# Kernel tuning notes

Measured on AMD Instinct MI355X. Metric: run time of the kernel, lower is better.

Reference implementation:

```python
import jax, jax.numpy as jnp
import numpy as np

OBS = 4096      # flattened observation size (hardcoded in down_sampler)
ENC = 1024      # encoding_size
LAT = 512       # policy_latent_size
ACT = 3         # action_space_n
B = 4096        # batch
NMAX = 8        # max neighbors (padded ragged dim)


def setup_inputs() -> dict:
    key = jax.random.key(0)
    ks = jax.random.split(key, 16)

    def w(i, shape, fan_in):
        return jax.random.normal(ks[i], shape, jnp.float32) * (1.0 / np.sqrt(fan_in))

    return {
        "observation": jax.random.normal(ks[0], (B, OBS), jnp.float32),
        "neighbors": jax.random.normal(ks[1], (B, NMAX, LAT), jnp.float32),
        "neighbor_counts": jax.random.randint(ks[2], (B,), 0, 9, jnp.int32),
        # down_sampler: Linear(4096, ENC) + ReLU
        "W_ds": w(3, (ENC, OBS), OBS), "b_ds": jnp.zeros((ENC,), jnp.float32),
        # policy: Linear(ENC, LAT) + ReLU
        "W_pol": w(4, (LAT, ENC), ENC), "b_pol": jnp.zeros((LAT,), jnp.float32),
        # v_net: Linear(ENC, 1) + Tanh
        "W_v": w(5, (1, ENC), ENC), "b_v": jnp.zeros((1,), jnp.float32),
        # GRUCell(LAT, LAT): weight_ih [3L, L], weight_hh [3L, L]
        "W_ih": w(6, (3 * LAT, LAT), LAT), "b_ih": jnp.zeros((3 * LAT,), jnp.float32),
        "W_hh": w(7, (3 * LAT, LAT), LAT), "b_hh": jnp.zeros((3 * LAT,), jnp.float32),
        # to_probs: Linear(LAT, ACT) + ReLU + Softmax
        "W_pr": w(8, (ACT, LAT), LAT), "b_pr": jnp.zeros((ACT,), jnp.float32),
    }


def _gru_cell(x, h, W_ih, b_ih, W_hh, b_hh):
    # PyTorch GRUCell semantics; gates ordered (r, z, n)
    gi = x @ W_ih.T + b_ih          # [B, 3L]
    gh = h @ W_hh.T + b_hh          # [B, 3L]
    i_r, i_z, i_n = jnp.split(gi, 3, axis=-1)
    h_r, h_z, h_n = jnp.split(gh, 3, axis=-1)
    r = jax.nn.sigmoid(i_r + h_r)
    z = jax.nn.sigmoid(i_z + h_z)
    n = jnp.tanh(i_n + r * h_n)
    return (1.0 - z) * n + z * h


def reference(observation, neighbors, neighbor_counts,
              W_ds, b_ds, W_pol, b_pol, W_v, b_v,
              W_ih, b_ih, W_hh, b_hh, W_pr, b_pr):
    # step 0: forward_initial
    enc = jax.nn.relu(observation @ W_ds.T + b_ds)        # [B, ENC]
    pol = jax.nn.relu(enc @ W_pol.T + b_pol)              # [B, LAT]
    state_vals = jnp.tanh(enc @ W_v.T + b_v)              # [B, 1]

    # step 1: forward_communicate -- ragged GRU recurrence over padded neighbors
    xs = jnp.swapaxes(neighbors, 0, 1)                    # [NMAX, B, LAT]
    ts = jnp.arange(NMAX)

    def step(h, xt):
        x, t = xt
        h_new = _gru_cell(x, h, W_ih, b_ih, W_hh, b_hh)
        valid = (t < neighbor_counts)[:, None]            # mask padded neighbor slots
        return jnp.where(valid, h_new, h), None

    h, _ = jax.lax.scan(step, pol, (xs, ts))              # [B, LAT]

    # step 2: forward_probs
    probs = jax.nn.softmax(jax.nn.relu(h @ W_pr.T + b_pr), axis=-1)  # [B, ACT]
    return probs, state_vals
```

## Files before the change

### kernel.cpp

```cpp
#include <hip/hip_runtime.h>
#include <hip/hip_bf16.h>

typedef __attribute__((ext_vector_type(8))) short short8;
typedef __attribute__((ext_vector_type(4))) float floatx4;

__device__ __forceinline__ ushort f2bf(float x) {
    unsigned u = __float_as_uint(x);
    unsigned r = (u + 0x7fffu + ((u >> 16) & 1u)) >> 16;
    return (ushort)r;
}
__device__ __forceinline__ float bf2f(ushort h) {
    return __uint_as_float(((unsigned)h) << 16);
}
__device__ __forceinline__ float fast_sigmoid(float x) {
    return 1.0f / (1.0f + __expf(-x));
}
__device__ __forceinline__ float fast_tanh(float x) {
    x = fminf(fmaxf(x, -15.0f), 15.0f);
    float e = __expf(2.0f * x);
    return (e - 1.0f) / (e + 1.0f);
}
__device__ __forceinline__ void load_lds16(const void* g, void* l) {
    __builtin_amdgcn_global_load_lds(
        (__attribute__((address_space(1))) void*)(g),
        (__attribute__((address_space(3))) void*)(l),
        16, 0, 0);
}

__device__ __forceinline__ void stage_unit(const ushort* grow0, int ld, ushort* lds_unit) {
    const int lane = threadIdx.x & 63;
    const int r = lane >> 3;
    const int c = (lane & 7) ^ r;
    load_lds16(grow0 + (size_t)r * ld + c * 8, lds_unit);
}
__device__ __forceinline__ short8 lds_read8(const ushort* buf, int R, int c_el) {
    const int idx = ((R >> 3) << 9) + ((R & 7) << 6) + ((((c_el >> 3) ^ (R & 7))) << 3);
    return *(const short8*)(buf + idx);
}

__global__ __launch_bounds__(256) void cvt_f32_bf16(const float* __restrict__ src,
                                                    ushort* __restrict__ dst, int n4) {
    int i = blockIdx.x * blockDim.x + threadIdx.x;
    if (i >= n4) return;
    const float4 v = ((const float4*)src)[i];
    ushort4 o;
    o.x = f2bf(v.x); o.y = f2bf(v.y); o.z = f2bf(v.z); o.w = f2bf(v.w);
    ((ushort4*)dst)[i] = o;
}

__global__ __launch_bounds__(256) void sort_by_cnt(const int* __restrict__ cnt,
                                                   int* __restrict__ perm,
                                                   int* __restrict__ inv,
                                                   int* __restrict__ nact) {
    __shared__ int h[9];
    __shared__ int cur[9];
    const int tid = threadIdx.x;
    if (tid < 9) h[tid] = 0;
    __syncthreads();
    for (int i = tid; i < 4096; i += 256) atomicAdd(&h[cnt[i]], 1);
    __syncthreads();
    if (tid == 0) {
        int off = 0;
        for (int c = 8; c >= 0; --c) { cur[c] = off; off += h[c]; }
        for (int t = 0; t < 8; ++t) {
            int n = 0;
            for (int c = t + 1; c <= 8; ++c) n += h[c];
            nact[t] = n;
        }
    }
    __syncthreads();
    for (int i = tid; i < 4096; i += 256) {
        const int c = cnt[i];
        const int p = atomicAdd(&cur[c], 1);
        perm[p] = i;
        inv[i] = p;
    }
}

template <int MODE, int BN, int KSPLIT, bool MAP>
__global__ __launch_bounds__(256, 2) void gemm64(
    const ushort* __restrict__ A, int lda,
    const ushort* __restrict__ B, int ldb,
    const float* __restrict__ bias,
    const int* __restrict__ row_map,
    ushort* __restrict__ Cb, float* __restrict__ Cf, int ldc,
    int K, size_t part_stride) {
    __shared__ __attribute__((aligned(16))) ushort sA[64 * 64];
    __shared__ __attribute__((aligned(16))) ushort sB[BN * 64];

    constexpr int NJ = (BN + 63) / 64;
    constexpr int UB = BN / 32;

    const int tid = threadIdx.x;
    const int lane = tid & 63;
    const int w = tid >> 6;
    const int m0 = blockIdx.y * 64;
    const int n0 = blockIdx.x * BN;
    const int wn = w * (16 * NJ);
    const int nl = lane & 15;

    const int Kper = K / KSPLIT;
    const int kbase = (KSPLIT > 1) ? blockIdx.z * Kper : 0;
    if (MODE == 3) Cf += (size_t)blockIdx.z * part_stride;

    floatx4 acc[4][NJ] = {};

    for (int k0 = kbase; k0 < kbase + Kper; k0 += 64) {
#pragma unroll
        for (int u = 0; u < 2; ++u) {
            const int ua = w * 2 + u;
            stage_unit(A + (size_t)(m0 + ua * 8) * lda + k0, lda, &sA[ua * 512]);
        }
#pragma unroll
        for (int u = 0; u < UB; ++u) {
            const int ub = w * UB + u;
            stage_unit(B + (size_t)(n0 + ub * 8) * ldb + k0, ldb, &sB[ub * 512]);
        }
        __syncthreads();
#pragma unroll
        for (int kk = 0; kk < 2; ++kk) {
            const int cb = kk * 32 + (lane >> 4) * 8;
            short8 a[4], b[NJ];
#pragma unroll
            for (int i = 0; i < 4; ++i) a[i] = lds_read8(sA, i * 16 + nl, cb);
#pragma unroll
            for (int j = 0; j < NJ; ++j) b[j] = lds_read8(sB, wn + j * 16 + nl, cb);
#pragma unroll
            for (int i = 0; i < 4; ++i)
#pragma unroll
                for (int j = 0; j < NJ; ++j)
                    acc[i][j] = __builtin_amdgcn_mfma_f32_16x16x32_bf16(a[i], b[j], acc[i][j], 0, 0, 0);
        }
        __syncthreads();
    }

    const int ml = (lane >> 4) * 4;
#pragma unroll
    for (int j = 0; j < NJ; ++j) {
        const int n = n0 + wn + j * 16 + nl;
        float bv = 0.0f;
        if (MODE == 2) bv = bias[n];
#pragma unroll
        for (int i = 0; i < 4; ++i) {
            const int mbase = m0 + i * 16 + ml;
#pragma unroll
            for (int r = 0; r < 4; ++r) {
                float v = acc[i][j][r];
                const int mr = mbase + r;
                const int orow = MAP ? row_map[mr] : mr;
                const size_t off = (size_t)orow * ldc + n;
                if (MODE == 2) {
                    v += bv; v = fmaxf(v, 0.0f);
                    Cb[off] = f2bf(v);
                    Cf[off] = v;
                } else {
                    Cf[off] = v;
                }
            }
        }
    }
}

__global__ __launch_bounds__(256) void combine_relu(const float* __restrict__ p0,
                                                    const float* __restrict__ p1,
                                                    const float* __restrict__ bias,
                                                    ushort* __restrict__ ob, int n4) {
    int i = blockIdx.x * blockDim.x + threadIdx.x;
    if (i >= n4) return;
    const float4 a = ((const float4*)p0)[i];
    const float4 b = ((const float4*)p1)[i];
    const int col = (i * 4) & 1023;
    const float4 bs = *(const float4*)(bias + col);
    ushort4 o;
    o.x = f2bf(fmaxf(a.x + b.x + bs.x, 0.f));
    o.y = f2bf(fmaxf(a.y + b.y + bs.y, 0.f));
    o.z = f2bf(fmaxf(a.z + b.z + bs.z, 0.f));
    o.w = f2bf(fmaxf(a.w + b.w + bs.w, 0.f));
    ((ushort4*)ob)[i] = o;
}

__global__ __launch_bounds__(256, 2) void gru_step(
    const ushort* __restrict__ Xall,
    const ushort* __restrict__ Hin,
    const ushort* __restrict__ Wih,
    const ushort* __restrict__ Whh,
    const float* __restrict__ bih, const float* __restrict__ bhh,
    const int* __restrict__ perm, const int* __restrict__ nact,
    float* __restrict__ hf, ushort* __restrict__ Hout, int t) {
    __shared__ __attribute__((aligned(16))) ushort sX[64 * 64];
    __shared__ __attribute__((aligned(16))) ushort sH[64 * 64];
    __shared__ __attribute__((aligned(16))) ushort sBih[192 * 64];
    __shared__ __attribute__((aligned(16))) ushort sBhh[192 * 64];

    const int tid = threadIdx.x;
    const int lane = tid & 63;
    const int w = tid >> 6;
    const int s = blockIdx.x;
    const int m0 = blockIdx.y * 64;
    const int na = nact[t];

    if (m0 >= na) {
        const int rr = tid >> 2;
        const size_t base = (size_t)(m0 + rr) * 512 + s * 64;
        const uint4* src = (const uint4*)(Hin + base);
        uint4* dst = (uint4*)(Hout + base);
        const int cc = (tid & 3) * 2;
        dst[cc] = src[cc];
        dst[cc + 1] = src[cc + 1];
        return;
    }

    const int nl = lane & 15;
    const int ml = (lane >> 4) * 4;
    const int col = s * 64 + w * 16 + nl;

    const int r = lane >> 3;
    const int c = (lane & 7) ^ r;
    const ushort* X = Xall + t * 512;
    const ushort* xb[2];
    const ushort* hbp[2];
#pragma unroll
    for (int u = 0; u < 2; ++u) {
        const int srow = m0 + (w * 2 + u) * 8 + r;
        const int orig = perm[srow];
        xb[u] = X + (size_t)orig * 4096 + c * 8;
        hbp[u] = Hin + (size_t)srow * 512 + c * 8;
    }
    const ushort* wi[6];
    const ushort* wh[6];
#pragma unroll
    for (int j = 0; j < 6; ++j) {
        const int u = w * 6 + j;
        const int grow = (u >> 3) * 512 + s * 64 + (u & 7) * 8 + r;
        wi[j] = Wih + (size_t)grow * 512 + c * 8;
        wh[j] = Whh + (size_t)grow * 512 + c * 8;
    }

    floatx4 accr[4], accz[4], accn[4], acch[4];
    {
        const float br_ = bih[col] + bhh[col];
        const float bz_ = bih[512 + col] + bhh[512 + col];
        const float bn_i = bih[1024 + col];
        const float bn_h = bhh[1024 + col];
        const floatx4 vr = {br_, br_, br_, br_};
        const floatx4 vz = {bz_, bz_, bz_, bz_};
        const floatx4 vi = {bn_i, bn_i, bn_i, bn_i};
        const floatx4 vh = {bn_h, bn_h, bn_h, bn_h};
#pragma unroll
        for (int i = 0; i < 4; ++i) { accr[i] = vr; accz[i] = vz; accn[i] = vi; acch[i] = vh; }
    }

    for (int k0 = 0; k0 < 512; k0 += 64) {
#pragma unroll
        for (int u = 0; u < 2; ++u) {
            const int ua = w * 2 + u;
            load_lds16(xb[u] + k0, &sX[ua * 512]);
            load_lds16(hbp[u] + k0, &sH[ua * 512]);
        }
#pragma unroll
        for (int j = 0; j < 6; ++j) {
            const int u = w * 6 + j;
            load_lds16(wi[j] + k0, &sBih[u * 512]);
            load_lds16(wh[j] + k0, &sBhh[u * 512]);
        }
        __syncthreads();
#pragma unroll
        for (int kk = 0; kk < 2; ++kk) {
            const int cb = kk * 32 + (lane >> 4) * 8;
            short8 ax[4], ah[4];
#pragma unroll
            for (int i = 0; i < 4; ++i) {
                ax[i] = lds_read8(sX, i * 16 + nl, cb);
                ah[i] = lds_read8(sH, i * 16 + nl, cb);
            }
            const short8 bir = lds_read8(sBih, w * 16 + nl, cb);
            const short8 biz = lds_read8(sBih, 64 + w * 16 + nl, cb);
            const short8 bin = lds_read8(sBih, 128 + w * 16 + nl, cb);
            const short8 bhr = lds_read8(sBhh, w * 16 + nl, cb);
            const short8 bhz = lds_read8(sBhh, 64 + w * 16 + nl, cb);
            const short8 bhn = lds_read8(sBhh, 128 + w * 16 + nl, cb);
#pragma unroll
            for (int i = 0; i < 4; ++i) {
                accr[i] = __builtin_amdgcn_mfma_f32_16x16x32_bf16(ax[i], bir, accr[i], 0, 0, 0);
                accr[i] = __builtin_amdgcn_mfma_f32_16x16x32_bf16(ah[i], bhr, accr[i], 0, 0, 0);
                accz[i] = __builtin_amdgcn_mfma_f32_16x16x32_bf16(ax[i], biz, accz[i], 0, 0, 0);
                accz[i] = __builtin_amdgcn_mfma_f32_16x16x32_bf16(ah[i], bhz, accz[i], 0, 0, 0);
                accn[i] = __builtin_amdgcn_mfma_f32_16x16x32_bf16(ax[i], bin, accn[i], 0, 0, 0);
                acch[i] = __builtin_amdgcn_mfma_f32_16x16x32_bf16(ah[i], bhn, acch[i], 0, 0, 0);
            }
        }
        __syncthreads();
    }

    const bool full = (m0 + 64 <= na);
#pragma unroll
    for (int i = 0; i < 4; ++i) {
#pragma unroll
        for (int r4 = 0; r4 < 4; ++r4) {
            const int lr = i * 16 + ml + r4;
            const int row = m0 + lr;
            const float rg = fast_sigmoid(accr[i][r4]);
            const float zg = fast_sigmoid(accz[i][r4]);
            const float ng = fast_tanh(accn[i][r4] + rg * acch[i][r4]);
            const size_t off = (size_t)row * 512 + col;
            const float ho = hf[off];
            const bool act = full || (row < na);
            const float hv = act ? ((1.0f - zg) * ng + zg * ho) : ho;
            hf[off] = hv;
            Hout[off] = f2bf(hv);
        }
    }
}

__global__ __launch_bounds__(256) void v_kernel(const ushort* __restrict__ enc,
                                                const float* __restrict__ Wv,
                                                const float* __restrict__ bv,
                                                float* __restrict__ out) {
    const int row = blockIdx.x * 4 + (threadIdx.x >> 6);
    const int lane = threadIdx.x & 63;
    const ushort* e = enc + (size_t)row * 1024;
    float s = 0.0f;
#pragma unroll
    for (int i = 0; i < 16; ++i) {
        int k = lane + i * 64;
        s += bf2f(e[k]) * Wv[k];
    }
#pragma unroll
    for (int off = 32; off; off >>= 1) s += __shfl_down(s, off, 64);
    if (lane == 0) out[row] = fast_tanh(s + bv[0]);
}

__global__ __launch_bounds__(256) void probs_kernel(const float* __restrict__ h,
                                                    const float* __restrict__ Wpr,
                                                    const float* __restrict__ bpr,
                                                    const int* __restrict__ perm,
                                                    float* __restrict__ out) {
    const int srow = blockIdx.x * 4 + (threadIdx.x >> 6);
    const int lane = threadIdx.x & 63;
    const float* hr = h + (size_t)srow * 512;
    float p0 = 0.f, p1 = 0.f, p2 = 0.f;
#pragma unroll
    for (int i = 0; i < 8; ++i) {
        int k = lane + i * 64;
        float x = hr[k];
        p0 += x * Wpr[k];
        p1 += x * Wpr[512 + k];
        p2 += x * Wpr[1024 + k];
    }
#pragma unroll
    for (int off = 32; off; off >>= 1) {
        p0 += __shfl_down(p0, off, 64);
        p1 += __shfl_down(p1, off, 64);
        p2 += __shfl_down(p2, off, 64);
    }
    if (lane == 0) {
        const int orow = perm[srow];
        p0 = fmaxf(p0 + bpr[0], 0.f);
        p1 = fmaxf(p1 + bpr[1], 0.f);
        p2 = fmaxf(p2 + bpr[2], 0.f);
        float m = fmaxf(p0, fmaxf(p1, p2));
        float e0 = __expf(p0 - m), e1 = __expf(p1 - m), e2 = __expf(p2 - m);
        float inv = 1.0f / (e0 + e1 + e2);
        out[orow * 3 + 0] = e0 * inv;
        out[orow * 3 + 1] = e1 * inv;
        out[orow * 3 + 2] = e2 * inv;
    }
}

extern "C" void kernel_launch(void* const* d_in, const int* in_sizes, int n_in,
                              void* d_out, int out_size, void* d_ws, size_t ws_size,
                              hipStream_t stream) {
    const float* obs   = (const float*)d_in[0];
    const float* nbr   = (const float*)d_in[1];
    const int*   cnt   = (const int*)d_in[2];
    const float* W_ds  = (const float*)d_in[3];
    const float* b_ds  = (const float*)d_in[4];
    const float* W_pol = (const float*)d_in[5];
    const float* b_pol = (const float*)d_in[6];
    const float* W_v   = (const float*)d_in[7];
    const float* b_v   = (const float*)d_in[8];
    const float* W_ih  = (const float*)d_in[9];
    const float* b_ih  = (const float*)d_in[10];
    const float* W_hh  = (const float*)d_in[11];
    const float* b_hh  = (const float*)d_in[12];
    const float* W_pr  = (const float*)d_in[13];
    const float* b_pr  = (const float*)d_in[14];
    float* out = (float*)d_out;

    ushort* obs_b  = (ushort*)d_ws;
    ushort* Wds_b  = obs_b + 16777216;
    ushort* Wpol_b = Wds_b + 4194304;
    ushort* Wih_b  = Wpol_b + 524288;
    ushort* Whh_b  = Wih_b + 786432;
    ushort* enc_b  = Whh_b + 786432;
    ushort* h_b0   = enc_b + 4194304;
    ushort* h_b1   = h_b0 + 2097152;
    float*  h_f    = (float*)(h_b1 + 2097152);
    float*  part   = h_f + 2097152;
    ushort* nbr_b  = (ushort*)part;
    int*    perm   = (int*)(part + 8388608);
    int*    inv    = perm + 4096;
    int*    nact   = inv + 4096;

    sort_by_cnt<<<1, 256, 0, stream>>>(cnt, perm, inv, nact);

    cvt_f32_bf16<<<16384, 256, 0, stream>>>(obs, obs_b, 4194304);
    cvt_f32_bf16<<<4096, 256, 0, stream>>>(W_ds, Wds_b, 1048576);
    cvt_f32_bf16<<<512, 256, 0, stream>>>(W_pol, Wpol_b, 131072);
    cvt_f32_bf16<<<768, 256, 0, stream>>>(W_ih, Wih_b, 196608);
    cvt_f32_bf16<<<768, 256, 0, stream>>>(W_hh, Whh_b, 196608);

    gemm64<3, 128, 2, false><<<dim3(8, 64, 2), 256, 0, stream>>>(
        obs_b, 4096, Wds_b, 4096, nullptr, nullptr, nullptr, part, 1024, 4096, 4194304);
    combine_relu<<<4096, 256, 0, stream>>>(part, part + 4194304, b_ds, enc_b, 1048576);

    cvt_f32_bf16<<<16384, 256, 0, stream>>>(nbr, nbr_b, 4194304);

    gemm64<2, 64, 1, true><<<dim3(8, 64, 1), 256, 0, stream>>>(
        enc_b, 1024, Wpol_b, 1024, b_pol, inv, h_b0, h_f, 512, 1024, 0);

    v_kernel<<<1024, 256, 0, stream>>>(enc_b, W_v, b_v, out + 12288);

    for (int t = 0; t < 8; ++t) {
        const ushort* hin = (t & 1) ? h_b1 : h_b0;
        ushort* hout = (t & 1) ? h_b0 : h_b1;
        gru_step<<<dim3(8, 64), 256, 0, stream>>>(nbr_b, hin, Wih_b, Whh_b,
                                                  b_ih, b_hh, perm, nact, h_f, hout, t);
    }

    probs_kernel<<<1024, 256, 0, stream>>>(h_f, W_pr, b_pr, perm, out);
}
```

Measured before the change: 440.8 us.

## Split GRU input projection into separate GEMM and drop split-K in encoder GEMM

The encoder GEMM stops using split-K with a separate combine/ReLU kernel. It now runs a single full-K pass that fuses bias, ReLU and the bf16 store, with a block-index swizzle to improve cache locality. The GRU step is split in two: a per-step gi_gemm computes the input projection into an fp32 buffer aliased over the dead obs workspace, and gru_step does only the hidden projection plus the gates, using less LDS and higher occupancy. This trades eight extra launches and fp32 gi traffic for lighter recurrent kernels and the removal of the partial-sum round trip.

New measurement: 506.1 us. +14.8%, slower.

```diff
diff --git a/kernel.cpp b/kernel.cpp
--- a/kernel.cpp
+++ b/kernel.cpp
@@ -77,35 +77,40 @@
     }
 }
 
-template <int MODE, int BN, int KSPLIT, bool MAP>
+template <int MODE, int BN, bool MAP, bool SWZ>
 __global__ __launch_bounds__(256, 2) void gemm64(
     const ushort* __restrict__ A, int lda,
     const ushort* __restrict__ B, int ldb,
     const float* __restrict__ bias,
     const int* __restrict__ row_map,
     ushort* __restrict__ Cb, float* __restrict__ Cf, int ldc,
-    int K, size_t part_stride) {
+    int K) {
     __shared__ __attribute__((aligned(16))) ushort sA[64 * 64];
     __shared__ __attribute__((aligned(16))) ushort sB[BN * 64];
 
     constexpr int NJ = (BN + 63) / 64;
     constexpr int UB = BN / 32;
+
+    int bx = blockIdx.x, by = blockIdx.y;
+    if (SWZ) {
+        const int nwg = gridDim.x * gridDim.y;
+        const int b = by * gridDim.x + bx;
+        const int f = (b & 7) * (nwg >> 3) + (b >> 3);
+        bx = f % gridDim.x;
+        by = f / gridDim.x;
+    }
 
     const int tid = threadIdx.x;
     const int lane = tid & 63;
     const int w = tid >> 6;
-    const int m0 = blockIdx.y * 64;
-    const int n0 = blockIdx.x * BN;
+    const int m0 = by * 64;
+    const int n0 = bx * BN;
     const int wn = w * (16 * NJ);
     const int nl = lane & 15;
 
-    const int Kper = K / KSPLIT;
-    const int kbase = (KSPLIT > 1) ? blockIdx.z * Kper : 0;
-    if (MODE == 3) Cf += (size_t)blockIdx.z * part_stride;
-
     floatx4 acc[4][NJ] = {};
 
-    for (int k0 = kbase; k0 < kbase + Kper; k0 += 64) {
+    for (int k0 = 0; k0 < K; k0 += 64) {
 #pragma unroll
         for (int u = 0; u < 2; ++u) {
             const int ua = w * 2 + u;
@@ -138,59 +143,105 @@
 #pragma unroll
     for (int j = 0; j < NJ; ++j) {
         const int n = n0 + wn + j * 16 + nl;
-        float bv = 0.0f;
-        if (MODE == 2) bv = bias[n];
+        const float bv = bias[n];
 #pragma unroll
         for (int i = 0; i < 4; ++i) {
             const int mbase = m0 + i * 16 + ml;
 #pragma unroll
             for (int r = 0; r < 4; ++r) {
-                float v = acc[i][j][r];
+                float v = acc[i][j][r] + bv;
+                v = fmaxf(v, 0.0f);
                 const int mr = mbase + r;
                 const int orow = MAP ? row_map[mr] : mr;
                 const size_t off = (size_t)orow * ldc + n;
-                if (MODE == 2) {
-                    v += bv; v = fmaxf(v, 0.0f);
-                    Cb[off] = f2bf(v);
-                    Cf[off] = v;
-                } else {
-                    Cf[off] = v;
-                }
+                Cb[off] = f2bf(v);
+                if (MODE == 2) Cf[off] = v;
             }
         }
     }
 }
 
-__global__ __launch_bounds__(256) void combine_relu(const float* __restrict__ p0,
-                                                    const float* __restrict__ p1,
-                                                    const float* __restrict__ bias,
-                                                    ushort* __restrict__ ob, int n4) {
-    int i = blockIdx.x * blockDim.x + threadIdx.x;
-    if (i >= n4) return;
-    const float4 a = ((const float4*)p0)[i];
-    const float4 b = ((const float4*)p1)[i];
-    const int col = (i * 4) & 1023;
-    const float4 bs = *(const float4*)(bias + col);
-    ushort4 o;
-    o.x = f2bf(fmaxf(a.x + b.x + bs.x, 0.f));
-    o.y = f2bf(fmaxf(a.y + b.y + bs.y, 0.f));
-    o.z = f2bf(fmaxf(a.z + b.z + bs.z, 0.f));
-    o.w = f2bf(fmaxf(a.w + b.w + bs.w, 0.f));
-    ((ushort4*)ob)[i] = o;
-}
-
-__global__ __launch_bounds__(256, 2) void gru_step(
+__global__ __launch_bounds__(256, 4) void gi_gemm(
     const ushort* __restrict__ Xall,
+    const ushort* __restrict__ Wih,
+    const float* __restrict__ bih,
+    const int* __restrict__ perm, const int* __restrict__ nact,
+    float* __restrict__ gi, int t) {
+    __shared__ __attribute__((aligned(16))) ushort sA[64 * 64];
+    __shared__ __attribute__((aligned(16))) ushort sB[128 * 64];
+
+    const int m0 = blockIdx.y * 64;
+    if (m0 >= nact[t]) return;
+
+    const int tid = threadIdx.x;
+    const int lane = tid & 63;
+    const int w = tid >> 6;
+    const int n0 = blockIdx.x * 128;
+    const int wn = w * 32;
+    const int nl = lane & 15;
+
+    const int r = lane >> 3;
+    const int c = (lane & 7) ^ r;
+    const ushort* xb[2];
+#pragma unroll
+    for (int u = 0; u < 2; ++u) {
+        const int srow = m0 + (w * 2 + u) * 8 + r;
+        xb[u] = Xall + (size_t)perm[srow] * 4096 + t * 512 + c * 8;
+    }
+
+    floatx4 acc[4][2] = {};
+
+    for (int k0 = 0; k0 < 512; k0 += 64) {
+#pragma unroll
+        for (int u = 0; u < 2; ++u) load_lds16(xb[u] + k0, &sA[(w * 2 + u) * 512]);
+#pragma unroll
+        for (int u = 0; u < 4; ++u) {
+            const int ub = w * 4 + u;
+            stage_unit(Wih + (size_t)(n0 + ub * 8) * 512 + k0, 512, &sB[ub * 512]);
+        }
+        __syncthreads();
+#pragma unroll
+        for (int kk = 0; kk < 2; ++kk) {
+            const int cb = kk * 32 + (lane >> 4) * 8;
+            short8 a[4], b[2];
+#pragma unroll
+            for (int i = 0; i < 4; ++i) a[i] = lds_read8(sA, i * 16 + nl, cb);
+#pragma unroll
+            for (int j = 0; j < 2; ++j) b[j] = lds_read8(sB, wn + j * 16 + nl, cb);
+#pragma unroll
+            for (int i = 0; i < 4; ++i)
+#pragma unroll
+                for (int j = 0; j < 2; ++j)
+                    acc[i][j] = __builtin_amdgcn_mfma_f32_16x16x32_bf16(a[i], b[j], acc[i][j], 0, 0, 0);
+        }
+        __syncthreads();
+    }
+
+    const int ml = (lane >> 4) * 4;
+#pragma unroll
+    for (int j = 0; j < 2; ++j) {
+        const int n = n0 + wn + j * 16 + nl;
+        const float bv = bih[n];
+#pragma unroll
+        for (int i = 0; i < 4; ++i) {
+#pragma unroll
+            for (int r4 = 0; r4 < 4; ++r4) {
+                const int row = m0 + i * 16 + ml + r4;
+                gi[(size_t)row * 1536 + n] = acc[i][j][r4] + bv;
+            }
+        }
+    }
+}
+
+__global__ __launch_bounds__(256, 4) void gru_step(
     const ushort* __restrict__ Hin,
-    const ushort* __restrict__ Wih,
     const ushort* __restrict__ Whh,
-    const float* __restrict__ bih, const float* __restrict__ bhh,
-    const int* __restrict__ perm, const int* __restrict__ nact,
+    const float* __restrict__ bhh,
+    const int* __restrict__ nact,
+    const float* __restrict__ gi,
     float* __restrict__ hf, ushort* __restrict__ Hout, int t) {
-    __shared__ __attribute__((aligned(16))) ushort sX[64 * 64];
     __shared__ __attribute__((aligned(16))) ushort sH[64 * 64];
-    __shared__ __attribute__((aligned(16))) ushort sBih[192 * 64];
-    __shared__ __attribute__((aligned(16))) ushort sBhh[192 * 64];
+    __shared__ __attribute__((aligned(16))) ushort sW[192 * 64];
 
     const int tid = threadIdx.x;
     const int lane = tid & 63;
@@ -216,76 +267,49 @@
 
     const int r = lane >> 3;
     const int c = (lane & 7) ^ r;
-    const ushort* X = Xall + t * 512;
-    const ushort* xb[2];
     const ushort* hbp[2];
 #pragma unroll
-    for (int u = 0; u < 2; ++u) {
-        const int srow = m0 + (w * 2 + u) * 8 + r;
-        const int orig = perm[srow];
-        xb[u] = X + (size_t)orig * 4096 + c * 8;
-        hbp[u] = Hin + (size_t)srow * 512 + c * 8;
-    }
-    const ushort* wi[6];
+    for (int u = 0; u < 2; ++u)
+        hbp[u] = Hin + (size_t)(m0 + (w * 2 + u) * 8 + r) * 512 + c * 8;
     const ushort* wh[6];
 #pragma unroll
     for (int j = 0; j < 6; ++j) {
         const int u = w * 6 + j;
         const int grow = (u >> 3) * 512 + s * 64 + (u & 7) * 8 + r;
-        wi[j] = Wih + (size_t)grow * 512 + c * 8;
         wh[j] = Whh + (size_t)grow * 512 + c * 8;
     }
 
-    floatx4 accr[4], accz[4], accn[4], acch[4];
+    floatx4 accr[4], accz[4], acch[4];
     {
-        const float br_ = bih[col] + bhh[col];
-        const float bz_ = bih[512 + col] + bhh[512 + col];
-        const float bn_i = bih[1024 + col];
-        const float bn_h = bhh[1024 + col];
+        const float br_ = bhh[col];
+        const float bz_ = bhh[512 + col];
+        const float bn_ = bhh[1024 + col];
         const floatx4 vr = {br_, br_, br_, br_};
         const floatx4 vz = {bz_, bz_, bz_, bz_};
-        const floatx4 vi = {bn_i, bn_i, bn_i, bn_i};
-        const floatx4 vh = {bn_h, bn_h, bn_h, bn_h};
-#pragma unroll
-        for (int i = 0; i < 4; ++i) { accr[i] = vr; accz[i] = vz; accn[i] = vi; acch[i] = vh; }
+        const floatx4 vh = {bn_, bn_, bn_, bn_};
+#pragma unroll
+        for (int i = 0; i < 4; ++i) { accr[i] = vr; accz[i] = vz; acch[i] = vh; }
     }
 
     for (int k0 = 0; k0 < 512; k0 += 64) {
 #pragma unroll
-        for (int u = 0; u < 2; ++u) {
-            const int ua = w * 2 + u;
-            load_lds16(xb[u] + k0, &sX[ua * 512]);
-            load_lds16(hbp[u] + k0, &sH[ua * 512]);
-        }
-#pragma unroll
-        for (int j = 0; j < 6; ++j) {
-            const int u = w * 6 + j;
-            load_lds16(wi[j] + k0, &sBih[u * 512]);
-            load_lds16(wh[j] + k0, &sBhh[u * 512]);
-        }
+        for (int u = 0; u < 2; ++u) load_lds16(hbp[u] + k0, &sH[(w * 2 + u) * 512]);
+#pragma unroll
+        for (int j = 0; j < 6; ++j) load_lds16(wh[j] + k0, &sW[(w * 6 + j) * 512]);
         __syncthreads();
 #pragma unroll
         for (int kk = 0; kk < 2; ++kk) {
             const int cb = kk * 32 + (lane >> 4) * 8;
-            short8 ax[4], ah[4];
+            short8 ah[4];
+#pragma unroll
+            for (int i = 0; i < 4; ++i) ah[i] = lds_read8(sH, i * 16 + nl, cb);
+            const short8 bhr = lds_read8(sW, w * 16 + nl, cb);
+            const short8 bhz = lds_read8(sW, 64 + w * 16 + nl, cb);
+            const short8 bhn = lds_read8(sW, 128 + w * 16 + nl, cb);
 #pragma unroll
             for (int i = 0; i < 4; ++i) {
-                ax[i] = lds_read8(sX, i * 16 + nl, cb);
-                ah[i] = lds_read8(sH, i * 16 + nl, cb);
-            }
-            const short8 bir = lds_read8(sBih, w * 16 + nl, cb);
-            const short8 biz = lds_read8(sBih, 64 + w * 16 + nl, cb);
-            const short8 bin = lds_read8(sBih, 128 + w * 16 + nl, cb);
-            const short8 bhr = lds_read8(sBhh, w * 16 + nl, cb);
-            const short8 bhz = lds_read8(sBhh, 64 + w * 16 + nl, cb);
-            const short8 bhn = lds_read8(sBhh, 128 + w * 16 + nl, cb);
-#pragma unroll
-            for (int i = 0; i < 4; ++i) {
-                accr[i] = __builtin_amdgcn_mfma_f32_16x16x32_bf16(ax[i], bir, accr[i], 0, 0, 0);
                 accr[i] = __builtin_amdgcn_mfma_f32_16x16x32_bf16(ah[i], bhr, accr[i], 0, 0, 0);
-                accz[i] = __builtin_amdgcn_mfma_f32_16x16x32_bf16(ax[i], biz, accz[i], 0, 0, 0);
                 accz[i] = __builtin_amdgcn_mfma_f32_16x16x32_bf16(ah[i], bhz, accz[i], 0, 0, 0);
-                accn[i] = __builtin_amdgcn_mfma_f32_16x16x32_bf16(ax[i], bin, accn[i], 0, 0, 0);
                 acch[i] = __builtin_amdgcn_mfma_f32_16x16x32_bf16(ah[i], bhn, acch[i], 0, 0, 0);
             }
         }
@@ -297,11 +321,14 @@
     for (int i = 0; i < 4; ++i) {
 #pragma unroll
         for (int r4 = 0; r4 < 4; ++r4) {
-            const int lr = i * 16 + ml + r4;
-            const int row = m0 + lr;
-            const float rg = fast_sigmoid(accr[i][r4]);
-            const float zg = fast_sigmoid(accz[i][r4]);
-            const float ng = fast_tanh(accn[i][r4] + rg * acch[i][r4]);
+            const int row = m0 + i * 16 + ml + r4;
+            const size_t gbase = (size_t)row * 1536;
+            const float gir = gi[gbase + col];
+            const float giz = gi[gbase + 512 + col];
+            const float gin = gi[gbase + 1024 + col];
+            const float rg = fast_sigmoid(gir + accr[i][r4]);
+            const float zg = fast_sigmoid(giz + accz[i][r4]);
+            const float ng = fast_tanh(gin + rg * acch[i][r4]);
             const size_t off = (size_t)row * 512 + col;
             const float ho = hf[off];
             const bool act = full || (row < na);
@@ -396,11 +423,11 @@
     ushort* h_b0   = enc_b + 4194304;
     ushort* h_b1   = h_b0 + 2097152;
     float*  h_f    = (float*)(h_b1 + 2097152);
-    float*  part   = h_f + 2097152;
-    ushort* nbr_b  = (ushort*)part;
-    int*    perm   = (int*)(part + 8388608);
+    ushort* nbr_b  = (ushort*)(h_f + 2097152);
+    int*    perm   = (int*)(nbr_b + 16777216);
     int*    inv    = perm + 4096;
     int*    nact   = inv + 4096;
+    float*  gi_f   = (float*)d_ws;
 
     sort_by_cnt<<<1, 256, 0, stream>>>(cnt, perm, inv, nact);
 
@@ -410,22 +437,21 @@
     cvt_f32_bf16<<<768, 256, 0, stream>>>(W_ih, Wih_b, 196608);
     cvt_f32_bf16<<<768, 256, 0, stream>>>(W_hh, Whh_b, 196608);
 
-    gemm64<3, 128, 2, false><<<dim3(8, 64, 2), 256, 0, stream>>>(
-        obs_b, 4096, Wds_b, 4096, nullptr, nullptr, nullptr, part, 1024, 4096, 4194304);
-    combine_relu<<<4096, 256, 0, stream>>>(part, part + 4194304, b_ds, enc_b, 1048576);
+    gemm64<4, 128, false, true><<<dim3(8, 64), 256, 0, stream>>>(
+        obs_b, 4096, Wds_b, 4096, b_ds, nullptr, enc_b, nullptr, 1024, 4096);
 
     cvt_f32_bf16<<<16384, 256, 0, stream>>>(nbr, nbr_b, 4194304);
 
-    gemm64<2, 64, 1, true><<<dim3(8, 64, 1), 256, 0, stream>>>(
-        enc_b, 1024, Wpol_b, 1024, b_pol, inv, h_b0, h_f, 512, 1024, 0);
+    gemm64<2, 64, true, false><<<dim3(8, 64), 256, 0, stream>>>(
+        enc_b, 1024, Wpol_b, 1024, b_pol, inv, h_b0, h_f, 512, 1024);
 
     v_kernel<<<1024, 256, 0, stream>>>(enc_b, W_v, b_v, out + 12288);
 
     for (int t = 0; t < 8; ++t) {
         const ushort* hin = (t & 1) ? h_b1 : h_b0;
         ushort* hout = (t & 1) ? h_b0 : h_b1;
-        gru_step<<<dim3(8, 64), 256, 0, stream>>>(nbr_b, hin, Wih_b, Whh_b,
-                                                  b_ih, b_hh, perm, nact, h_f, hout, t);
+        gi_gemm<<<dim3(12, 64), 256, 0, stream>>>(nbr_b, Wih_b, b_ih, perm, nact, gi_f, t);
+        gru_step<<<dim3(8, 64), 256, 0, stream>>>(hin, Whh_b, b_hh, nact, gi_f, h_f, hout, t);
     }
 
     probs_kernel<<<1024, 256, 0, stream>>>(h_f, W_pr, b_pr, perm, out);
```

## Fuse GRU steps into persistent kernel with grid barriers; merge conversions; swizzle GEMM

Applied to the files above, without the earlier changes.

Replaces the eight per-timestep GRU launches with one persistent kernel of 512 blocks. Each block keeps its fp32 hidden state in registers, exchanges bf16 hidden state through global ping-pong buffers and synchronises with atomic grid barriers. The five fp32-to-bf16 conversion launches become a single kernel, and the large down-sampler GEMM gets a block-index swizzle meant to improve L2 reuse. The aim is to cut launch overhead, skip the inactive-block copies and avoid per-step fp32 state traffic. The cost is that all 512 blocks must be co-resident, and the spin barrier, which has a timeout, risks hangs or silent wrong results if they are not.

New measurement: 1.427 ms. +223.7%, slower.

```diff
diff --git a/kernel.cpp b/kernel.cpp
--- a/kernel.cpp
+++ b/kernel.cpp
@@ -36,6 +36,42 @@
 __device__ __forceinline__ short8 lds_read8(const ushort* buf, int R, int c_el) {
     const int idx = ((R >> 3) << 9) + ((R & 7) << 6) + ((((c_el >> 3) ^ (R & 7))) << 3);
     return *(const short8*)(buf + idx);
+}
+
+__device__ __forceinline__ void grid_barrier(int* cnt, int target) {
+    __syncthreads();
+    if (threadIdx.x == 0) {
+        __threadfence();
+        __hip_atomic_fetch_add(cnt, 1, __ATOMIC_RELEASE, __HIP_MEMORY_SCOPE_AGENT);
+        long spins = 0;
+        while (__hip_atomic_load(cnt, __ATOMIC_ACQUIRE, __HIP_MEMORY_SCOPE_AGENT) < target) {
+            if (++spins > (1L << 23)) break;
+        }
+        __threadfence();
+    }
+    __syncthreads();
+}
+
+__global__ __launch_bounds__(256) void cvt_all(
+    const float* __restrict__ s0, ushort* __restrict__ d0,
+    const float* __restrict__ s1, ushort* __restrict__ d1,
+    const float* __restrict__ s2, ushort* __restrict__ d2,
+    const float* __restrict__ s3, ushort* __restrict__ d3,
+    const float* __restrict__ s4, ushort* __restrict__ d4) {
+    int i = blockIdx.x * 256 + threadIdx.x;
+    const float* s;
+    ushort* d;
+    int j;
+    if (i < 4194304)      { s = s0; d = d0; j = i; }
+    else if (i < 5242880) { s = s1; d = d1; j = i - 4194304; }
+    else if (i < 5373952) { s = s2; d = d2; j = i - 5242880; }
+    else if (i < 5570560) { s = s3; d = d3; j = i - 5373952; }
+    else if (i < 5767168) { s = s4; d = d4; j = i - 5570560; }
+    else return;
+    const float4 v = ((const float4*)s)[j];
+    ushort4 o;
+    o.x = f2bf(v.x); o.y = f2bf(v.y); o.z = f2bf(v.z); o.w = f2bf(v.w);
+    ((ushort4*)d)[j] = o;
 }
 
 __global__ __launch_bounds__(256) void cvt_f32_bf16(const float* __restrict__ src,
@@ -51,11 +87,13 @@
 __global__ __launch_bounds__(256) void sort_by_cnt(const int* __restrict__ cnt,
                                                    int* __restrict__ perm,
                                                    int* __restrict__ inv,
-                                                   int* __restrict__ nact) {
+                                                   int* __restrict__ nact,
+                                                   int* __restrict__ bar) {
     __shared__ int h[9];
     __shared__ int cur[9];
     const int tid = threadIdx.x;
     if (tid < 9) h[tid] = 0;
+    if (tid < 8) bar[tid] = 0;
     __syncthreads();
     for (int i = tid; i < 4096; i += 256) atomicAdd(&h[cnt[i]], 1);
     __syncthreads();
@@ -77,7 +115,7 @@
     }
 }
 
-template <int MODE, int BN, int KSPLIT, bool MAP>
+template <int MODE, int BN, int KSPLIT, bool MAP, bool SWZ>
 __global__ __launch_bounds__(256, 2) void gemm64(
     const ushort* __restrict__ A, int lda,
     const ushort* __restrict__ B, int ldb,
@@ -91,11 +129,20 @@
     constexpr int NJ = (BN + 63) / 64;
     constexpr int UB = BN / 32;
 
+    int bx = blockIdx.x, by = blockIdx.y;
+    if (SWZ) {
+        const int nwg = gridDim.x * gridDim.y;
+        const int b = by * gridDim.x + bx;
+        const int f = (b & 7) * (nwg >> 3) + (b >> 3);
+        bx = f % gridDim.x;
+        by = f / gridDim.x;
+    }
+
     const int tid = threadIdx.x;
     const int lane = tid & 63;
     const int w = tid >> 6;
-    const int m0 = blockIdx.y * 64;
-    const int n0 = blockIdx.x * BN;
+    const int m0 = by * 64;
+    const int n0 = bx * BN;
     const int wn = w * (16 * NJ);
     const int nl = lane & 15;
 
@@ -179,14 +226,16 @@
     ((ushort4*)ob)[i] = o;
 }
 
-__global__ __launch_bounds__(256, 2) void gru_step(
+__global__ __launch_bounds__(256, 2) void gru_persistent(
     const ushort* __restrict__ Xall,
-    const ushort* __restrict__ Hin,
     const ushort* __restrict__ Wih,
     const ushort* __restrict__ Whh,
     const float* __restrict__ bih, const float* __restrict__ bhh,
     const int* __restrict__ perm, const int* __restrict__ nact,
-    float* __restrict__ hf, ushort* __restrict__ Hout, int t) {
+    const float* __restrict__ h0f,
+    ushort* __restrict__ Hg0, ushort* __restrict__ Hg1,
+    float* __restrict__ hf_out,
+    int* __restrict__ bar) {
     __shared__ __attribute__((aligned(16))) ushort sX[64 * 64];
     __shared__ __attribute__((aligned(16))) ushort sH[64 * 64];
     __shared__ __attribute__((aligned(16))) ushort sBih[192 * 64];
@@ -195,36 +244,28 @@
     const int tid = threadIdx.x;
     const int lane = tid & 63;
     const int w = tid >> 6;
-    const int s = blockIdx.x;
-    const int m0 = blockIdx.y * 64;
-    const int na = nact[t];
-
-    if (m0 >= na) {
-        const int rr = tid >> 2;
-        const size_t base = (size_t)(m0 + rr) * 512 + s * 64;
-        const uint4* src = (const uint4*)(Hin + base);
-        uint4* dst = (uint4*)(Hout + base);
-        const int cc = (tid & 3) * 2;
-        dst[cc] = src[cc];
-        dst[cc + 1] = src[cc + 1];
-        return;
-    }
-
+    const int s = blockIdx.x & 7;
+    const int m0 = (blockIdx.x >> 3) * 64;
     const int nl = lane & 15;
     const int ml = (lane >> 4) * 4;
     const int col = s * 64 + w * 16 + nl;
 
+    float hreg[4][4];
+#pragma unroll
+    for (int i = 0; i < 4; ++i)
+#pragma unroll
+        for (int r4 = 0; r4 < 4; ++r4)
+            hreg[i][r4] = h0f[(size_t)(m0 + i * 16 + ml + r4) * 512 + col];
+
     const int r = lane >> 3;
     const int c = (lane & 7) ^ r;
-    const ushort* X = Xall + t * 512;
     const ushort* xb[2];
-    const ushort* hbp[2];
+    size_t hoff[2];
 #pragma unroll
     for (int u = 0; u < 2; ++u) {
         const int srow = m0 + (w * 2 + u) * 8 + r;
-        const int orig = perm[srow];
-        xb[u] = X + (size_t)orig * 4096 + c * 8;
-        hbp[u] = Hin + (size_t)srow * 512 + c * 8;
+        xb[u] = Xall + (size_t)perm[srow] * 4096 + c * 8;
+        hoff[u] = (size_t)srow * 512 + c * 8;
     }
     const ushort* wi[6];
     const ushort* wh[6];
@@ -235,81 +276,95 @@
         wi[j] = Wih + (size_t)grow * 512 + c * 8;
         wh[j] = Whh + (size_t)grow * 512 + c * 8;
     }
-
-    floatx4 accr[4], accz[4], accn[4], acch[4];
-    {
-        const float br_ = bih[col] + bhh[col];
-        const float bz_ = bih[512 + col] + bhh[512 + col];
-        const float bn_i = bih[1024 + col];
-        const float bn_h = bhh[1024 + col];
-        const floatx4 vr = {br_, br_, br_, br_};
-        const floatx4 vz = {bz_, bz_, bz_, bz_};
-        const floatx4 vi = {bn_i, bn_i, bn_i, bn_i};
-        const floatx4 vh = {bn_h, bn_h, bn_h, bn_h};
-#pragma unroll
-        for (int i = 0; i < 4; ++i) { accr[i] = vr; accz[i] = vz; accn[i] = vi; acch[i] = vh; }
-    }
-
-    for (int k0 = 0; k0 < 512; k0 += 64) {
-#pragma unroll
-        for (int u = 0; u < 2; ++u) {
-            const int ua = w * 2 + u;
-            load_lds16(xb[u] + k0, &sX[ua * 512]);
-            load_lds16(hbp[u] + k0, &sH[ua * 512]);
-        }
-#pragma unroll
-        for (int j = 0; j < 6; ++j) {
-            const int u = w * 6 + j;
-            load_lds16(wi[j] + k0, &sBih[u * 512]);
-            load_lds16(wh[j] + k0, &sBhh[u * 512]);
-        }
-        __syncthreads();
-#pragma unroll
-        for (int kk = 0; kk < 2; ++kk) {
-            const int cb = kk * 32 + (lane >> 4) * 8;
-            short8 ax[4], ah[4];
-#pragma unroll
-            for (int i = 0; i < 4; ++i) {
-                ax[i] = lds_read8(sX, i * 16 + nl, cb);
-                ah[i] = lds_read8(sH, i * 16 + nl, cb);
+    const float br_ = bih[col] + bhh[col];
+    const float bz_ = bih[512 + col] + bhh[512 + col];
+    const float bni = bih[1024 + col];
+    const float bnh = bhh[1024 + col];
+
+    for (int t = 0; t < 8; ++t) {
+        const int na = nact[t];
+        const ushort* Hin = (t & 1) ? Hg1 : Hg0;
+        ushort* Hout = (t & 1) ? Hg0 : Hg1;
+        const bool active = (m0 < na);
+        if (active) {
+            floatx4 accr[4], accz[4], accn[4], acch[4];
+            {
+                const floatx4 vr = {br_, br_, br_, br_};
+                const floatx4 vz = {bz_, bz_, bz_, bz_};
+                const floatx4 vi = {bni, bni, bni, bni};
+                const floatx4 vh = {bnh, bnh, bnh, bnh};
+#pragma unroll
+                for (int i = 0; i < 4; ++i) { accr[i] = vr; accz[i] = vz; accn[i] = vi; acch[i] = vh; }
             }
-            const short8 bir = lds_read8(sBih, w * 16 + nl, cb);
-            const short8 biz = lds_read8(sBih, 64 + w * 16 + nl, cb);
-            const short8 bin = lds_read8(sBih, 128 + w * 16 + nl, cb);
-            const short8 bhr = lds_read8(sBhh, w * 16 + nl, cb);
-            const short8 bhz = lds_read8(sBhh, 64 + w * 16 + nl, cb);
-            const short8 bhn = lds_read8(sBhh, 128 + w * 16 + nl, cb);
-#pragma unroll
-            for (int i = 0; i < 4; ++i) {
-                accr[i] = __builtin_amdgcn_mfma_f32_16x16x32_bf16(ax[i], bir, accr[i], 0, 0, 0);
-                accr[i] = __builtin_amdgcn_mfma_f32_16x16x32_bf16(ah[i], bhr, accr[i], 0, 0, 0);
-                accz[i] = __builtin_amdgcn_mfma_f32_16x16x32_bf16(ax[i], biz, accz[i], 0, 0, 0);
-                accz[i] = __builtin_amdgcn_mfma_f32_16x16x32_bf16(ah[i], bhz, accz[i], 0, 0, 0);
-                accn[i] = __builtin_amdgcn_mfma_f32_16x16x32_bf16(ax[i], bin, accn[i], 0, 0, 0);
-                acch[i] = __builtin_amdgcn_mfma_f32_16x16x32_bf16(ah[i], bhn, acch[i], 0, 0, 0);
+            for (int k0 = 0; k0 < 512; k0 += 64) {
+#pragma unroll
+                for (int u = 0; u < 2; ++u) {
+                    const int ua = w * 2 + u;
+                    load_lds16(xb[u] + t * 512 + k0, &sX[ua * 512]);
+                    load_lds16(Hin + hoff[u] + k0, &sH[ua * 512]);
+                }
+#pragma unroll
+                for (int j = 0; j < 6; ++j) {
+                    const int u = w * 6 + j;
+                    load_lds16(wi[j] + k0, &sBih[u * 512]);
+                    load_lds16(wh[j] + k0, &sBhh[u * 512]);
+                }
+                __syncthreads();
+#pragma unroll
+                for (int kk = 0; kk < 2; ++kk) {
+                    const int cb = kk * 32 + (lane >> 4) * 8;
+                    short8 ax[4], ah[4];
+#pragma unroll
+                    for (int i = 0; i < 4; ++i) {
+                        ax[i] = lds_read8(sX, i * 16 + nl, cb);
+                        ah[i] = lds_read8(sH, i * 16 + nl, cb);
+                    }
+                    const short8 bir = lds_read8(sBih, w * 16 + nl, cb);
+                    const short8 biz = lds_read8(sBih, 64 + w * 16 + nl, cb);
+                    const short8 bin = lds_read8(sBih, 128 + w * 16 + nl, cb);
+                    const short8 bhr = lds_read8(sBhh, w * 16 + nl, cb);
+                    const short8 bhz = lds_read8(sBhh, 64 + w * 16 + nl, cb);
+                    const short8 bhn = lds_read8(sBhh, 128 + w * 16 + nl, cb);
+#pragma unroll
+                    for (int i = 0; i < 4; ++i) {
+                        accr[i] = __builtin_amdgcn_mfma_f32_16x16x32_bf16(ax[i], bir, accr[i], 0, 0, 0);
+                        accr[i] = __builtin_amdgcn_mfma_f32_16x16x32_bf16(ah[i], bhr, accr[i], 0, 0, 0);
+                        accz[i] = __builtin_amdgcn_mfma_f32_16x16x32_bf16(ax[i], biz, accz[i], 0, 0, 0);
+                        accz[i] = __builtin_amdgcn_mfma_f32_16x16x32_bf16(ah[i], bhz, accz[i], 0, 0, 0);
+                        accn[i] = __builtin_amdgcn_mfma_f32_16x16x32_bf16(ax[i], bin, accn[i], 0, 0, 0);
+                        acch[i] = __builtin_amdgcn_mfma_f32_16x16x32_bf16(ah[i], bhn, acch[i], 0, 0, 0);
+                    }
+                }
+                __syncthreads();
             }
-        }
-        __syncthreads();
-    }
-
-    const bool full = (m0 + 64 <= na);
-#pragma unroll
-    for (int i = 0; i < 4; ++i) {
-#pragma unroll
-        for (int r4 = 0; r4 < 4; ++r4) {
-            const int lr = i * 16 + ml + r4;
-            const int row = m0 + lr;
-            const float rg = fast_sigmoid(accr[i][r4]);
-            const float zg = fast_sigmoid(accz[i][r4]);
-            const float ng = fast_tanh(accn[i][r4] + rg * acch[i][r4]);
-            const size_t off = (size_t)row * 512 + col;
-            const float ho = hf[off];
-            const bool act = full || (row < na);
-            const float hv = act ? ((1.0f - zg) * ng + zg * ho) : ho;
-            hf[off] = hv;
-            Hout[off] = f2bf(hv);
-        }
-    }
+            const bool full = (m0 + 64 <= na);
+#pragma unroll
+            for (int i = 0; i < 4; ++i)
+#pragma unroll
+                for (int r4 = 0; r4 < 4; ++r4) {
+                    const int row = m0 + i * 16 + ml + r4;
+                    const float rg = fast_sigmoid(accr[i][r4]);
+                    const float zg = fast_sigmoid(accz[i][r4]);
+                    const float ng = fast_tanh(accn[i][r4] + rg * acch[i][r4]);
+                    if (full || row < na)
+                        hreg[i][r4] = (1.0f - zg) * ng + zg * hreg[i][r4];
+                }
+            if (t < 7) {
+#pragma unroll
+                for (int i = 0; i < 4; ++i)
+#pragma unroll
+                    for (int r4 = 0; r4 < 4; ++r4)
+                        Hout[(size_t)(m0 + i * 16 + ml + r4) * 512 + col] = f2bf(hreg[i][r4]);
+            }
+        }
+        if (t < 7) grid_barrier(&bar[t], 512);
+    }
+
+#pragma unroll
+    for (int i = 0; i < 4; ++i)
+#pragma unroll
+        for (int r4 = 0; r4 < 4; ++r4)
+            hf_out[(size_t)(m0 + i * 16 + ml + r4) * 512 + col] = hreg[i][r4];
 }
 
 __global__ __launch_bounds__(256) void v_kernel(const ushort* __restrict__ enc,
@@ -401,32 +456,26 @@
     int*    perm   = (int*)(part + 8388608);
     int*    inv    = perm + 4096;
     int*    nact   = inv + 4096;
-
-    sort_by_cnt<<<1, 256, 0, stream>>>(cnt, perm, inv, nact);
-
-    cvt_f32_bf16<<<16384, 256, 0, stream>>>(obs, obs_b, 4194304);
-    cvt_f32_bf16<<<4096, 256, 0, stream>>>(W_ds, Wds_b, 1048576);
-    cvt_f32_bf16<<<512, 256, 0, stream>>>(W_pol, Wpol_b, 131072);
-    cvt_f32_bf16<<<768, 256, 0, stream>>>(W_ih, Wih_b, 196608);
-    cvt_f32_bf16<<<768, 256, 0, stream>>>(W_hh, Whh_b, 196608);
-
-    gemm64<3, 128, 2, false><<<dim3(8, 64, 2), 256, 0, stream>>>(
+    int*    bar    = nact + 16;
+
+    sort_by_cnt<<<1, 256, 0, stream>>>(cnt, perm, inv, nact, bar);
+
+    cvt_all<<<22528, 256, 0, stream>>>(obs, obs_b, W_ds, Wds_b, W_pol, Wpol_b,
+                                       W_ih, Wih_b, W_hh, Whh_b);
+
+    gemm64<3, 128, 2, false, true><<<dim3(8, 64, 2), 256, 0, stream>>>(
         obs_b, 4096, Wds_b, 4096, nullptr, nullptr, nullptr, part, 1024, 4096, 4194304);
     combine_relu<<<4096, 256, 0, stream>>>(part, part + 4194304, b_ds, enc_b, 1048576);
 
     cvt_f32_bf16<<<16384, 256, 0, stream>>>(nbr, nbr_b, 4194304);
 
-    gemm64<2, 64, 1, true><<<dim3(8, 64, 1), 256, 0, stream>>>(
+    gemm64<2, 64, 1, true, false><<<dim3(8, 64, 1), 256, 0, stream>>>(
         enc_b, 1024, Wpol_b, 1024, b_pol, inv, h_b0, h_f, 512, 1024, 0);
 
     v_kernel<<<1024, 256, 0, stream>>>(enc_b, W_v, b_v, out + 12288);
 
-    for (int t = 0; t < 8; ++t) {
-        const ushort* hin = (t & 1) ? h_b1 : h_b0;
-        ushort* hout = (t & 1) ? h_b0 : h_b1;
-        gru_step<<<dim3(8, 64), 256, 0, stream>>>(nbr_b, hin, Wih_b, Whh_b,
-                                                  b_ih, b_hh, perm, nact, h_f, hout, t);
-    }
+    gru_persistent<<<dim3(512), 256, 0, stream>>>(
+        nbr_b, Wih_b, Whh_b, b_ih, b_hh, perm, nact, h_f, h_b0, h_b1, h_f, bar);
 
     probs_kernel<<<1024, 256, 0, stream>>>(h_f, W_pr, b_pr, perm, out);
 }
```

## Widen GRU step tiles to 128 rows and fuse fp32-to-bf16 conversion launches

Applied to the files above, without the earlier changes.

The GRU step kernel now uses 512-thread blocks covering 128 batch rows, with two row groups of waves. This halves the number of times each block's weight slice is staged from global memory into LDS, and it uses dynamic shared memory sized for the larger tile. Blocks whose rows are all inactive now exit without copying the bf16 hidden state forward, and the final step skips writing the bf16 hidden copy. The five separate conversion launches are merged into one kernel that branches on index range. The larger tile needs 80 KB of LDS per block, which may limit occupancy or latency hiding.

Measured after the change: 474.4 us. +7.6%, slower.

```diff
diff --git a/kernel.cpp b/kernel.cpp
--- a/kernel.cpp
+++ b/kernel.cpp
@@ -36,6 +36,28 @@
 __device__ __forceinline__ short8 lds_read8(const ushort* buf, int R, int c_el) {
     const int idx = ((R >> 3) << 9) + ((R & 7) << 6) + ((((c_el >> 3) ^ (R & 7))) << 3);
     return *(const short8*)(buf + idx);
+}
+
+__global__ __launch_bounds__(256) void cvt_all(
+    const float* __restrict__ s0, ushort* __restrict__ d0,
+    const float* __restrict__ s1, ushort* __restrict__ d1,
+    const float* __restrict__ s2, ushort* __restrict__ d2,
+    const float* __restrict__ s3, ushort* __restrict__ d3,
+    const float* __restrict__ s4, ushort* __restrict__ d4) {
+    int i = blockIdx.x * 256 + threadIdx.x;
+    const float* s;
+    ushort* d;
+    int j;
+    if (i < 4194304)      { s = s0; d = d0; j = i; }
+    else if (i < 5242880) { s = s1; d = d1; j = i - 4194304; }
+    else if (i < 5373952) { s = s2; d = d2; j = i - 5242880; }
+    else if (i < 5570560) { s = s3; d = d3; j = i - 5373952; }
+    else if (i < 5767168) { s = s4; d = d4; j = i - 5570560; }
+    else return;
+    const float4 v = ((const float4*)s)[j];
+    ushort4 o;
+    o.x = f2bf(v.x); o.y = f2bf(v.y); o.z = f2bf(v.z); o.w = f2bf(v.w);
+    ((ushort4*)d)[j] = o;
 }
 
 __global__ __launch_bounds__(256) void cvt_f32_bf16(const float* __restrict__ src,
@@ -179,7 +201,7 @@
     ((ushort4*)ob)[i] = o;
 }
 
-__global__ __launch_bounds__(256, 2) void gru_step(
+__global__ __launch_bounds__(512, 2) void gru_step(
     const ushort* __restrict__ Xall,
     const ushort* __restrict__ Hin,
     const ushort* __restrict__ Wih,
@@ -187,51 +209,44 @@
     const float* __restrict__ bih, const float* __restrict__ bhh,
     const int* __restrict__ perm, const int* __restrict__ nact,
     float* __restrict__ hf, ushort* __restrict__ Hout, int t) {
-    __shared__ __attribute__((aligned(16))) ushort sX[64 * 64];
-    __shared__ __attribute__((aligned(16))) ushort sH[64 * 64];
-    __shared__ __attribute__((aligned(16))) ushort sBih[192 * 64];
-    __shared__ __attribute__((aligned(16))) ushort sBhh[192 * 64];
+    extern __shared__ __attribute__((aligned(16))) ushort smem[];
+    ushort* sX   = smem;
+    ushort* sH   = sX + 8192;
+    ushort* sBih = sH + 8192;
+    ushort* sBhh = sBih + 12288;
 
     const int tid = threadIdx.x;
     const int lane = tid & 63;
     const int w = tid >> 6;
+    const int wr = w >> 2;
+    const int wc = w & 3;
     const int s = blockIdx.x;
-    const int m0 = blockIdx.y * 64;
+    const int m0 = blockIdx.y * 128;
     const int na = nact[t];
-
-    if (m0 >= na) {
-        const int rr = tid >> 2;
-        const size_t base = (size_t)(m0 + rr) * 512 + s * 64;
-        const uint4* src = (const uint4*)(Hin + base);
-        uint4* dst = (uint4*)(Hout + base);
-        const int cc = (tid & 3) * 2;
-        dst[cc] = src[cc];
-        dst[cc + 1] = src[cc + 1];
-        return;
-    }
+    if (m0 >= na) return;
 
     const int nl = lane & 15;
     const int ml = (lane >> 4) * 4;
-    const int col = s * 64 + w * 16 + nl;
+    const int col = s * 64 + wc * 16 + nl;
 
     const int r = lane >> 3;
     const int c = (lane & 7) ^ r;
-    const ushort* X = Xall + t * 512;
     const ushort* xb[2];
     const ushort* hbp[2];
 #pragma unroll
     for (int u = 0; u < 2; ++u) {
-        const int srow = m0 + (w * 2 + u) * 8 + r;
+        const int ua = w * 2 + u;
+        const int srow = m0 + ua * 8 + r;
         const int orig = perm[srow];
-        xb[u] = X + (size_t)orig * 4096 + c * 8;
+        xb[u] = Xall + (size_t)orig * 4096 + t * 512 + c * 8;
         hbp[u] = Hin + (size_t)srow * 512 + c * 8;
     }
-    const ushort* wi[6];
-    const ushort* wh[6];
-#pragma unroll
-    for (int j = 0; j < 6; ++j) {
-        const int u = w * 6 + j;
-        const int grow = (u >> 3) * 512 + s * 64 + (u & 7) * 8 + r;
+    const ushort* wi[3];
+    const ushort* wh[3];
+#pragma unroll
+    for (int j = 0; j < 3; ++j) {
+        const int uw = w * 3 + j;
+        const int grow = (uw >> 3) * 512 + s * 64 + (uw & 7) * 8 + r;
         wi[j] = Wih + (size_t)grow * 512 + c * 8;
         wh[j] = Whh + (size_t)grow * 512 + c * 8;
     }
@@ -258,10 +273,10 @@
             load_lds16(hbp[u] + k0, &sH[ua * 512]);
         }
 #pragma unroll
-        for (int j = 0; j < 6; ++j) {
-            const int u = w * 6 + j;
-            load_lds16(wi[j] + k0, &sBih[u * 512]);
-            load_lds16(wh[j] + k0, &sBhh[u * 512]);
+        for (int j = 0; j < 3; ++j) {
+            const int uw = w * 3 + j;
+            load_lds16(wi[j] + k0, &sBih[uw * 512]);
+            load_lds16(wh[j] + k0, &sBhh[uw * 512]);
         }
         __syncthreads();
 #pragma unroll
@@ -270,15 +285,15 @@
             short8 ax[4], ah[4];
 #pragma unroll
             for (int i = 0; i < 4; ++i) {
-                ax[i] = lds_read8(sX, i * 16 + nl, cb);
-                ah[i] = lds_read8(sH, i * 16 + nl, cb);
+                ax[i] = lds_read8(sX, wr * 64 + i * 16 + nl, cb);
+                ah[i] = lds_read8(sH, wr * 64 + i * 16 + nl, cb);
             }
-            const short8 bir = lds_read8(sBih, w * 16 + nl, cb);
-            const short8 biz = lds_read8(sBih, 64 + w * 16 + nl, cb);
-            const short8 bin = lds_read8(sBih, 128 + w * 16 + nl, cb);
-            const short8 bhr = lds_read8(sBhh, w * 16 + nl, cb);
-            const short8 bhz = lds_read8(sBhh, 64 + w * 16 + nl, cb);
-            const short8 bhn = lds_read8(sBhh, 128 + w * 16 + nl, cb);
+            const short8 bir = lds_read8(sBih, wc * 16 + nl, cb);
+            const short8 biz = lds_read8(sBih, 64 + wc * 16 + nl, cb);
+            const short8 bin = lds_read8(sBih, 128 + wc * 16 + nl, cb);
+            const short8 bhr = lds_read8(sBhh, wc * 16 + nl, cb);
+            const short8 bhz = lds_read8(sBhh, 64 + wc * 16 + nl, cb);
+            const short8 bhn = lds_read8(sBhh, 128 + wc * 16 + nl, cb);
 #pragma unroll
             for (int i = 0; i < 4; ++i) {
                 accr[i] = __builtin_amdgcn_mfma_f32_16x16x32_bf16(ax[i], bir, accr[i], 0, 0, 0);
@@ -292,13 +307,13 @@
         __syncthreads();
     }
 
-    const bool full = (m0 + 64 <= na);
+    const bool full = (m0 + 128 <= na);
+    const int rbase = m0 + wr * 64;
 #pragma unroll
     for (int i = 0; i < 4; ++i) {
 #pragma unroll
         for (int r4 = 0; r4 < 4; ++r4) {
-            const int lr = i * 16 + ml + r4;
-            const int row = m0 + lr;
+            const int row = rbase + i * 16 + ml + r4;
             const float rg = fast_sigmoid(accr[i][r4]);
             const float zg = fast_sigmoid(accz[i][r4]);
             const float ng = fast_tanh(accn[i][r4] + rg * acch[i][r4]);
@@ -307,7 +322,7 @@
             const bool act = full || (row < na);
             const float hv = act ? ((1.0f - zg) * ng + zg * ho) : ho;
             hf[off] = hv;
-            Hout[off] = f2bf(hv);
+            if (t < 7) Hout[off] = f2bf(hv);
         }
     }
 }
@@ -402,13 +417,17 @@
     int*    inv    = perm + 4096;
     int*    nact   = inv + 4096;
 
+    static bool attr_done = false;
+    if (!attr_done) {
+        hipFuncSetAttribute((const void*)gru_step,
+                            hipFuncAttributeMaxDynamicSharedMemorySize, 81920);
+        attr_done = true;
+    }
+
     sort_by_cnt<<<1, 256, 0, stream>>>(cnt, perm, inv, nact);
 
-    cvt_f32_bf16<<<16384, 256, 0, stream>>>(obs, obs_b, 4194304);
-    cvt_f32_bf16<<<4096, 256, 0, stream>>>(W_ds, Wds_b, 1048576);
-    cvt_f32_bf16<<<512, 256, 0, stream>>>(W_pol, Wpol_b, 131072);
-    cvt_f32_bf16<<<768, 256, 0, stream>>>(W_ih, Wih_b, 196608);
-    cvt_f32_bf16<<<768, 256, 0, stream>>>(W_hh, Whh_b, 196608);
+    cvt_all<<<22528, 256, 0, stream>>>(obs, obs_b, W_ds, Wds_b, W_pol, Wpol_b,
+                                       W_ih, Wih_b, W_hh, Whh_b);
 
     gemm64<3, 128, 2, false><<<dim3(8, 64, 2), 256, 0, stream>>>(
         obs_b, 4096, Wds_b, 4096, nullptr, nullptr, nullptr, part, 1024, 4096, 4194304);
@@ -424,8 +443,8 @@
     for (int t = 0; t < 8; ++t) {
         const ushort* hin = (t & 1) ? h_b1 : h_b0;
         ushort* hout = (t & 1) ? h_b0 : h_b1;
-        gru_step<<<dim3(8, 64), 256, 0, stream>>>(nbr_b, hin, Wih_b, Whh_b,
-                                                  b_ih, b_hh, perm, nact, h_f, hout, t);
+        gru_step<<<dim3(8, 32), 512, 81920, stream>>>(nbr_b, hin, Wih_b, Whh_b,
+                                                      b_ih, b_hh, perm, nact, h_f, hout, t);
     }
 
     probs_kernel<<<1024, 256, 0, stream>>>(h_f, W_pr, b_pr, perm, out);
```
